# Performance work log

Measured on AMD Instinct MI355X. Metric: run time of the kernel, lower is better.

## Reference

```python
import jax, jax.numpy as jnp
import numpy as np
import math

N, E, G = 10000, 100000, 500
HID, H = 128, 4
C = HID                      # out_channels per head (PyG TransformerConv)
NFREQ, NSPACE = 10, 3
EDIM = 2 * NFREQ * NSPACE    # 60 = dis_emb.dim
LAT, DIS = 6, 3
IN_DIM = HID + LAT + DIS     # 137
EPS = 1e-5


def _lin_init(k, fan_in, shape):
    b = 1.0 / math.sqrt(fan_in)
    return jax.random.uniform(k, shape, jnp.float32, -b, b)


def setup_inputs() -> dict:
    key = jax.random.key(0)
    ks = jax.random.split(key, 12)
    return dict(
        node_features=jax.random.normal(ks[0], (N, HID), jnp.float32),
        frac_coords=jax.random.uniform(ks[1], (N, DIS), jnp.float32),
        lattice_feats=jax.random.normal(ks[2], (G, LAT), jnp.float32),
        edge_index=jax.random.randint(ks[3], (2, E), 0, N),
        node2graph=jnp.sort(jax.random.randint(ks[4], (N,), 0, G)),
        frac_diff=jax.random.normal(ks[5], (E, DIS), jnp.float32) * 0.1,
        ln_gamma=jnp.ones((HID,), jnp.float32),
        ln_beta=jnp.zeros((HID,), jnp.float32),
        Wq=_lin_init(ks[6], IN_DIM, (IN_DIM, H * C)), bq=jnp.zeros((H * C,), jnp.float32),
        Wk=_lin_init(ks[7], IN_DIM, (IN_DIM, H * C)), bk=jnp.zeros((H * C,), jnp.float32),
        Wv=_lin_init(ks[8], IN_DIM, (IN_DIM, H * C)), bv=jnp.zeros((H * C,), jnp.float32),
        We=_lin_init(ks[9], EDIM, (EDIM, H * C)),
        Wskip=_lin_init(ks[10], IN_DIM, (IN_DIM, C)), bskip=jnp.zeros((C,), jnp.float32),
    )


def _sinusoids(frac_diff):
    # SinusoidsEmbedding: emb = x[...,None]*2*pi*arange(F); cat(sin, cos); detached
    freqs = 2.0 * jnp.pi * jnp.arange(NFREQ, dtype=jnp.float32)    # [F]
    emb = frac_diff[:, :, None] * freqs[None, None, :]             # [E,3,F]
    emb = emb.reshape(-1, NSPACE * NFREQ)                          # [E,30]
    return jnp.concatenate([jnp.sin(emb), jnp.cos(emb)], axis=-1)  # [E,60]


def _segment_softmax(scores, idx, num_segments):
    # softmax over variable-size neighborhoods grouped by target node idx
    m = jax.ops.segment_max(scores, idx, num_segments=num_segments)
    ex = jnp.exp(scores - m[idx])
    s = jax.ops.segment_sum(ex, idx, num_segments=num_segments)
    return ex / (s[idx] + 1e-16)


def reference(node_features, frac_coords, lattice_feats, edge_index, node2graph,
              frac_diff, ln_gamma, ln_beta, Wq, bq, Wk, bk, Wv, bv, We, Wskip, bskip):
    edge_emb = jax.lax.stop_gradient(_sinusoids(frac_diff))  # .detach() in original
    node_input = node_features
    # LayerNorm (biased variance, torch default)
    mu = node_features.mean(-1, keepdims=True)
    var = node_features.var(-1, keepdims=True)
    h = (node_features - mu) * jax.lax.rsqrt(var + EPS) * ln_gamma + ln_beta
    # gather per-graph lattice features to nodes, concat
    lat = lattice_feats.reshape(-1, LAT)[node2graph]                # [N,6]
    x = jnp.concatenate([h, lat, frac_coords], axis=1)              # [N,137]

    q = (x @ Wq + bq).reshape(N, H, C)
    k = (x @ Wk + bk).reshape(N, H, C)
    v = (x @ Wv + bv).reshape(N, H, C)
    e = (edge_emb @ We).reshape(E, H, C)                            # lin_edge (no bias)

    src, dst = edge_index[0], edge_index[1]  # message flows src -> dst (PyG default)
    k_e = k[src] + e                                                # [E,H,C]
    alpha = (q[dst] * k_e).sum(-1) / math.sqrt(C)                   # [E,H]
    alpha = _segment_softmax(alpha, dst, N)
    msg = (v[src] + e) * alpha[:, :, None]                          # [E,H,C]
    out = jax.ops.segment_sum(msg, dst, num_segments=N)             # [N,H,C]
    out = out.mean(axis=1)                                          # concat=False -> head mean
    out = out + (x @ Wskip + bskip)                                 # root skip connection
    return node_input + jax.nn.silu(out)
```

## Files before the change

### kernel.cpp

```cpp
#include <hip/hip_runtime.h>
#include <math.h>

#define N_NODES 10000
#define N_EDGES 100000
#define HIDDEN  128
#define NHEAD   4
#define CHAN    128
#define IN_DIM  137
#define KPAD    160
#define NCOLS   1904
#define NPAD    1920
#define LATD    6
#define DISD    3

#define PREP_BLOCKS 2500
#define TRANS_TILES 26
#define WQE_BLOCKS  150
#define WEBT_BLOCKS 128

#define SCAT_BLOCKS ((N_EDGES + 255) / 256)
#define GEMM_BX 15
#define GEMM_BY ((N_NODES + 63) / 64)

typedef __attribute__((ext_vector_type(8))) short short8v;
typedef __attribute__((ext_vector_type(4))) float float4v;
typedef __attribute__((ext_vector_type(2))) float float2v;

__device__ inline unsigned short f2bf(float f) {
    unsigned u = __float_as_uint(f);
    unsigned r = 0x7fffu + ((u >> 16) & 1u);
    return (unsigned short)((u + r) >> 16);
}
__device__ inline float bf2f(unsigned short u) {
    return __uint_as_float(((unsigned)u) << 16);
}

__global__ __launch_bounds__(256) void prep_weights_kernel(
    const float* __restrict__ nf, const float* __restrict__ frac,
    const float* __restrict__ lat, const int* __restrict__ n2g,
    const float* __restrict__ gamma, const float* __restrict__ beta,
    const float* __restrict__ Wq, const float* __restrict__ bq,
    const float* __restrict__ Wk, const float* __restrict__ bk,
    const float* __restrict__ Wv, const float* __restrict__ bv,
    const float* __restrict__ Wsk, const float* __restrict__ bsk,
    const float* __restrict__ We,
    unsigned short* __restrict__ xb, int* __restrict__ hist,
    unsigned short* __restrict__ wallT, float* __restrict__ bias_all,
    unsigned short* __restrict__ webt)
{
    __shared__ __align__(16) unsigned short Tlds[64 * 168];
    const int tid = threadIdx.x;

    if (blockIdx.x < PREP_BLOCKS) {
        int wave = tid >> 6;
        int lane = tid & 63;
        int n = blockIdx.x * 4 + wave;
        if (n >= N_NODES) return;

        float v0 = nf[n * HIDDEN + lane];
        float v1 = nf[n * HIDDEN + 64 + lane];
        float s  = v0 + v1;
        float sq = v0 * v0 + v1 * v1;
        #pragma unroll
        for (int m = 1; m < 64; m <<= 1) {
            s  += __shfl_xor(s, m);
            sq += __shfl_xor(sq, m);
        }
        float mean = s * (1.0f / 128.0f);
        float var  = sq * (1.0f / 128.0f) - mean * mean;
        float inv  = rsqrtf(var + 1e-5f);

        xb[n * KPAD + lane]      = f2bf((v0 - mean) * inv * gamma[lane]      + beta[lane]);
        xb[n * KPAD + 64 + lane] = f2bf((v1 - mean) * inv * gamma[64 + lane] + beta[64 + lane]);
        if (lane < LATD) xb[n * KPAD + HIDDEN + lane]        = f2bf(lat[n2g[n] * LATD + lane]);
        if (lane < DISD) xb[n * KPAD + HIDDEN + LATD + lane] = f2bf(frac[n * DISD + lane]);
        if (lane >= 41)  xb[n * KPAD + 96 + lane] = 0;
        if (lane == 0)   hist[n] = 0;
    } else if (blockIdx.x < PREP_BLOCKS + TRANS_TILES) {
        const int n0 = (blockIdx.x - PREP_BLOCKS) * 64;
        for (int i = tid; i < 160 * 64; i += 256) {
            const int k = i >> 6, n = i & 63;
            const int col = n0 + n;
            float val = 0.0f;
            if (k < IN_DIM) {
                if (col < 512)        val = Wq[(size_t)k * 512 + col];
                else if (col < 1024)  val = Wk[(size_t)k * 512 + (col - 512)];
                else if (col < 1536)  val = Wv[(size_t)k * 512 + (col - 1024)];
                else                  val = Wsk[(size_t)k * 128 + (col - 1536)];
            }
            Tlds[n * 168 + k] = f2bf(val);
        }
        __syncthreads();
        for (int i = tid; i < 64 * 20; i += 256) {
            const int n = i / 20, c8 = (i % 20) * 8;
            *reinterpret_cast<uint4*>(&wallT[(size_t)(n0 + n) * KPAD + c8]) =
                *reinterpret_cast<const uint4*>(&Tlds[n * 168 + c8]);
        }
        if (tid < 64) {
            const int col = n0 + tid;
            float b;
            if (col < 512)        b = bq[col];
            else if (col < 1024)  b = bk[col - 512];
            else if (col < 1536)  b = bv[col - 1024];
            else                  b = bsk[col - 1536];
            bias_all[col] = b;
        }
    } else if (blockIdx.x < PREP_BLOCKS + TRANS_TILES + WQE_BLOCKS) {
        int idx = (blockIdx.x - PREP_BLOCKS - TRANS_TILES) * 256 + tid;
        if (idx >= 240 * KPAD) return;
        int hj = idx / KPAD, k = idx % KPAD;
        int h = hj / 60, j = hj % 60;
        float s = 0.0f;
        if (k < IN_DIM) {
            #pragma unroll 4
            for (int c = 0; c < 128; ++c)
                s += Wq[(size_t)k * 512 + h * 128 + c] * We[(size_t)j * 512 + h * 128 + c];
        }
        wallT[(size_t)(1664 + hj) * KPAD + k] = f2bf(s);
        if (k == KPAD - 1) {
            float b = 0.0f;
            #pragma unroll 4
            for (int c = 0; c < 128; ++c)
                b += bq[h * 128 + c] * We[(size_t)j * 512 + h * 128 + c];
            bias_all[1664 + hj] = b;
        }
    } else {
        int g = (blockIdx.x - PREP_BLOCKS - TRANS_TILES - WQE_BLOCKS) * 256 + tid;
        if (g >= 4 * 128 * 64) return;
        int h = g >> 13, c = (g >> 6) & 127, j = g & 63;
        float v = (j < 60) ? We[(size_t)j * 512 + h * 128 + c] : 0.0f;
        webt[g] = f2bf(v);
    }
}

__global__ __launch_bounds__(256) void hist_kernel(
    const int* __restrict__ eidx, int* __restrict__ hist)
{
    int e = blockIdx.x * 256 + threadIdx.x;
    if (e < N_EDGES) atomicAdd(&hist[eidx[N_EDGES + e]], 1);
}

__global__ __launch_bounds__(1024) void scan_kernel(
    const int* __restrict__ hist, int* __restrict__ offsets, int* __restrict__ cursor)
{
    __shared__ int part[1024];
    const int t = threadIdx.x;
    const int base = t * 10;
    int loc[10];
    int s = 0;
    #pragma unroll
    for (int i = 0; i < 10; ++i) {
        int v = (base + i < N_NODES) ? hist[base + i] : 0;
        loc[i] = s; s += v;
    }
    part[t] = s;
    __syncthreads();
    for (int off = 1; off < 1024; off <<= 1) {
        int v = (t >= off) ? part[t - off] : 0;
        __syncthreads();
        part[t] += v;
        __syncthreads();
    }
    int pre = (t > 0) ? part[t - 1] : 0;
    #pragma unroll
    for (int i = 0; i < 10; ++i)
        if (base + i < N_NODES) {
            offsets[base + i] = pre + loc[i];
            cursor[base + i]  = pre + loc[i];
        }
    if (t == 1023) offsets[N_NODES] = part[1023];
}

__global__ __launch_bounds__(256) void gemm_scatter_kernel(
    const unsigned short* __restrict__ xb, const unsigned short* __restrict__ wallT,
    const float* __restrict__ bias_all,
    const int* __restrict__ eidx, const float* __restrict__ fdiff,
    int* __restrict__ cursor, int* __restrict__ sorted_src,
    float* __restrict__ sorted_fd,
    float* __restrict__ sq, unsigned short* __restrict__ qbuf,
    unsigned char* __restrict__ kvb)
{
    __shared__ __align__(16) unsigned short Alds[64 * 168];

    if (blockIdx.x < SCAT_BLOCKS) {
        int e = blockIdx.x * 256 + threadIdx.x;
        if (e >= N_EDGES) return;
        int src = eidx[e];
        int dst = eidx[N_EDGES + e];
        int pos = atomicAdd(&cursor[dst], 1);
        sorted_src[pos] = src;
        sorted_fd[pos * 3 + 0] = fdiff[e * 3 + 0];
        sorted_fd[pos * 3 + 1] = fdiff[e * 3 + 1];
        sorted_fd[pos * 3 + 2] = fdiff[e * 3 + 2];
        return;
    }

    const int bx   = blockIdx.x - SCAT_BLOCKS;
    const int row0 = (bx / GEMM_BX) * 64;
    const int col0 = (bx % GEMM_BX) * 128;
    const int tid  = threadIdx.x;

    for (int i = tid; i < 64 * 20; i += 256) {
        int r = i / 20, c8 = (i % 20) * 8;
        uint4 v = make_uint4(0u, 0u, 0u, 0u);
        if (row0 + r < N_NODES)
            v = *reinterpret_cast<const uint4*>(&xb[(size_t)(row0 + r) * KPAD + c8]);
        *reinterpret_cast<uint4*>(&Alds[r * 168 + c8]) = v;
    }
    __syncthreads();

    const int l   = tid & 63;
    const int wid = tid >> 6;
    const int wr  = (wid >> 1) * 32;
    const int wc  = (wid & 1) * 64;
    const int lr  = l & 15;
    const int lk  = (l >> 4) * 8;

    float4v acc[2][4];
    #pragma unroll
    for (int tr = 0; tr < 2; ++tr)
        #pragma unroll
        for (int tc = 0; tc < 4; ++tc)
            acc[tr][tc] = (float4v){0.0f, 0.0f, 0.0f, 0.0f};

    #pragma unroll
    for (int ks = 0; ks < 5; ++ks) {
        short8v a[2], b[4];
        #pragma unroll
        for (int t = 0; t < 2; ++t)
            a[t] = *reinterpret_cast<const short8v*>(&Alds[(wr + t * 16 + lr) * 168 + ks * 32 + lk]);
        #pragma unroll
        for (int t = 0; t < 4; ++t)
            b[t] = *reinterpret_cast<const short8v*>(
                &wallT[(size_t)(col0 + wc + t * 16 + lr) * KPAD + ks * 32 + lk]);
        #pragma unroll
        for (int tr = 0; tr < 2; ++tr)
            #pragma unroll
            for (int tc = 0; tc < 4; ++tc)
                acc[tr][tc] = __builtin_amdgcn_mfma_f32_16x16x32_bf16(a[tr], b[tc], acc[tr][tc], 0, 0, 0);
    }

    #pragma unroll
    for (int tr = 0; tr < 2; ++tr) {
        #pragma unroll
        for (int tc = 0; tc < 4; ++tc) {
            const int col  = col0 + wc + tc * 16 + lr;
            const float bias = bias_all[col];
            #pragma unroll
            for (int j = 0; j < 4; ++j) {
                const int row = row0 + wr + tr * 16 + (l >> 4) * 4 + j;
                if (row < N_NODES) {
                    float val = acc[tr][tc][j] + bias;
                    if (col < 512) {
                        qbuf[(size_t)row * 512 + col] = f2bf(val);
                    } else if (col < 1024) {
                        const int h = (col - 512) >> 7, ck = (col - 512) & 127;
                        int p = __builtin_amdgcn_cvt_pk_fp8_f32(val, val, 0, false);
                        kvb[((size_t)row * 4 + h) * 256 + ck] = (unsigned char)(p & 0xFF);
                    } else if (col < 1536) {
                        const int h = (col - 1024) >> 7, cv = (col - 1024) & 127;
                        int p = __builtin_amdgcn_cvt_pk_fp8_f32(val, val, 0, false);
                        kvb[((size_t)row * 4 + h) * 256 + 128 + cv] = (unsigned char)(p & 0xFF);
                    } else if (col < 1664) {
                        sq[(size_t)row * 384 + (col - 1536)] = val;
                    } else if (col < NCOLS) {
                        sq[(size_t)row * 384 + 128 + (col - 1664)] = val;
                    }
                }
            }
        }
    }
}

__global__ __launch_bounds__(256) void gather_kernel(
    const float* __restrict__ sq, const unsigned short* __restrict__ qbuf,
    const unsigned char* __restrict__ kvb,
    const int* __restrict__ offsets, const int* __restrict__ sorted_src,
    const float* __restrict__ sorted_fd,
    float* __restrict__ avbuf, unsigned short* __restrict__ aggbuf,
    float* __restrict__ sumwbuf)
{
    const int n    = blockIdx.x;
    const int h    = threadIdx.x >> 6;
    const int l    = threadIdx.x & 63;
    const int hl   = l & 31;
    const int half = l >> 5;
    const float TWO_PI = 6.283185307179586f;
    const float scale  = 0.08838834764831845f;

    const ushort4 qv = *reinterpret_cast<const ushort4*>(
        &qbuf[(size_t)n * 512 + h * 128 + 4 * hl]);
    const float q4x = bf2f(qv.x), q4y = bf2f(qv.y);
    const float q4z = bf2f(qv.z), q4w = bf2f(qv.w);
    const float qe_a = sq[(size_t)n * 384 + 128 + h * 60 + hl];
    const bool  v2ok = (hl < 28);
    const float qe_b = v2ok ? sq[(size_t)n * 384 + 128 + h * 60 + hl + 32] : 0.0f;

    const int   jj1  = (hl < 30) ? hl : hl - 30;
    const int   sd1  = jj1 / 10;
    const float fc1  = TWO_PI * (float)(jj1 % 10);
    const bool  sin1 = (hl < 30);
    const int   jj2  = hl + 2;
    const int   sd2  = v2ok ? (jj2 / 10) : 0;
    const float fc2  = v2ok ? TWO_PI * (float)(jj2 % 10) : 0.0f;

    float ax = 0.f, ay = 0.f, az = 0.f, aw = 0.f;
    float agg1 = 0.f, agg2 = 0.f, sumw = 0.f;
    const int e0 = offsets[n], e1 = offsets[n + 1];

    for (int base = e0; base < e1; base += 4) {
        const int eA = base + half;
        const int eB = base + half + 2;
        const bool okA = (eA < e1), okB = (eB < e1);
        const int iA = okA ? eA : e0;
        const int iB = okB ? eB : e0;
        const int srcA = sorted_src[iA];
        const int srcB = sorted_src[iB];
        const float fdA1 = sorted_fd[iA * 3 + sd1];
        const float fdA2 = sorted_fd[iA * 3 + sd2];
        const float fdB1 = sorted_fd[iB * 3 + sd1];
        const float fdB2 = sorted_fd[iB * 3 + sd2];
        const unsigned char* pA = kvb + ((size_t)srcA * 4 + h) * 256;
        const unsigned char* pB = kvb + ((size_t)srcB * 4 + h) * 256;
        const unsigned kAu = *reinterpret_cast<const unsigned*>(pA + 4 * hl);
        const unsigned vAu = *reinterpret_cast<const unsigned*>(pA + 128 + 4 * hl);
        const unsigned kBu = *reinterpret_cast<const unsigned*>(pB + 4 * hl);
        const unsigned vBu = *reinterpret_cast<const unsigned*>(pB + 128 + 4 * hl);

        const float eA1 = sin1 ? __sinf(fdA1 * fc1) : __cosf(fdA1 * fc1);
        const float eA2 = __cosf(fdA2 * fc2);
        const float eB1 = sin1 ? __sinf(fdB1 * fc1) : __cosf(fdB1 * fc1);
        const float eB2 = __cosf(fdB2 * fc2);

        const float2v kA01 = __builtin_amdgcn_cvt_pk_f32_fp8(kAu, false);
        const float2v kA23 = __builtin_amdgcn_cvt_pk_f32_fp8(kAu, true);
        const float2v kB01 = __builtin_amdgcn_cvt_pk_f32_fp8(kBu, false);
        const float2v kB23 = __builtin_amdgcn_cvt_pk_f32_fp8(kBu, true);

        float pAs = q4x * kA01[0] + q4y * kA01[1]
                  + q4z * kA23[0] + q4w * kA23[1]
                  + eA1 * qe_a + eA2 * qe_b;
        float pBs = q4x * kB01[0] + q4y * kB01[1]
                  + q4z * kB23[0] + q4w * kB23[1]
                  + eB1 * qe_a + eB2 * qe_b;
        #pragma unroll
        for (int m = 1; m <= 16; m <<= 1) {
            pAs += __shfl_xor(pAs, m);
            pBs += __shfl_xor(pBs, m);
        }
        const float wA = okA ? __expf(pAs * scale) : 0.0f;
        const float wB = okB ? __expf(pBs * scale) : 0.0f;
        sumw += wA + wB;

        const float2v vA01 = __builtin_amdgcn_cvt_pk_f32_fp8(vAu, false);
        const float2v vA23 = __builtin_amdgcn_cvt_pk_f32_fp8(vAu, true);
        const float2v vB01 = __builtin_amdgcn_cvt_pk_f32_fp8(vBu, false);
        const float2v vB23 = __builtin_amdgcn_cvt_pk_f32_fp8(vBu, true);
        ax += wA * vA01[0] + wB * vB01[0];
        ay += wA * vA01[1] + wB * vB01[1];
        az += wA * vA23[0] + wB * vB23[0];
        aw += wA * vA23[1] + wB * vB23[1];
        agg1 += wA * eA1 + wB * eB1;
        if (v2ok) agg2 += wA * eA2 + wB * eB2;
    }

    sumw += __shfl_xor(sumw, 32);
    ax += __shfl_xor(ax, 32);  ay += __shfl_xor(ay, 32);
    az += __shfl_xor(az, 32);  aw += __shfl_xor(aw, 32);
    agg1 += __shfl_xor(agg1, 32);
    agg2 += __shfl_xor(agg2, 32);

    if (half == 0) {
        float4 r;
        r.x = ax; r.y = ay; r.z = az; r.w = aw;
        *reinterpret_cast<float4*>(&avbuf[(size_t)n * 512 + h * 128 + 4 * hl]) = r;
        aggbuf[n * 256 + h * 64 + hl]      = f2bf(agg1);
        aggbuf[n * 256 + h * 64 + 32 + hl] = f2bf(agg2);
        if (hl == 0) sumwbuf[n * 4 + h] = sumw;
    }
}

__global__ __launch_bounds__(256) void corr_kernel(
    const unsigned short* __restrict__ webt, const unsigned short* __restrict__ aggbuf,
    float* __restrict__ avbuf)
{
    __shared__ __align__(16) unsigned short Alds[32 * 264];
    const int node0 = blockIdx.x * 32;
    const int tid = threadIdx.x;

    for (int i = tid; i < 32 * 32; i += 256) {
        int r = i >> 5, c8 = (i & 31) * 8;
        uint4 v = make_uint4(0u, 0u, 0u, 0u);
        if (node0 + r < N_NODES)
            v = *reinterpret_cast<const uint4*>(&aggbuf[(size_t)(node0 + r) * 256 + c8]);
        *reinterpret_cast<uint4*>(&Alds[r * 264 + c8]) = v;
    }
    __syncthreads();

    const int l  = tid & 63;
    const int h  = tid >> 6;
    const int lr = l & 15;
    const int lk = (l >> 4) * 8;

    float4v acc[2][8];
    #pragma unroll
    for (int m = 0; m < 2; ++m)
        #pragma unroll
        for (int nn = 0; nn < 8; ++nn)
            acc[m][nn] = (float4v){0.0f, 0.0f, 0.0f, 0.0f};

    #pragma unroll
    for (int ks = 0; ks < 2; ++ks) {
        short8v a[2], b[8];
        #pragma unroll
        for (int m = 0; m < 2; ++m)
            a[m] = *reinterpret_cast<const short8v*>(
                &Alds[(m * 16 + lr) * 264 + h * 64 + ks * 32 + lk]);
        #pragma unroll
        for (int nn = 0; nn < 8; ++nn)
            b[nn] = *reinterpret_cast<const short8v*>(
                &webt[(size_t)(h * 128 + nn * 16 + lr) * 64 + ks * 32 + lk]);
        #pragma unroll
        for (int m = 0; m < 2; ++m)
            #pragma unroll
            for (int nn = 0; nn < 8; ++nn)
                acc[m][nn] = __builtin_amdgcn_mfma_f32_16x16x32_bf16(a[m], b[nn], acc[m][nn], 0, 0, 0);
    }

    #pragma unroll
    for (int m = 0; m < 2; ++m) {
        #pragma unroll
        for (int nn = 0; nn < 8; ++nn) {
            const int col = h * 128 + nn * 16 + lr;
            #pragma unroll
            for (int j = 0; j < 4; ++j) {
                const int rowi = node0 + m * 16 + (l >> 4) * 4 + j;
                if (rowi < N_NODES) {
                    float* p = &avbuf[(size_t)rowi * 512 + col];
                    *p += acc[m][nn][j];
                }
            }
        }
    }
}

__global__ __launch_bounds__(256) void finalize_kernel(
    const float* __restrict__ avbuf, const float* __restrict__ sumwbuf,
    const float* __restrict__ sq, const float* __restrict__ nf,
    float* __restrict__ out)
{
    int idx = blockIdx.x * 256 + threadIdx.x;
    if (idx >= N_NODES * CHAN) return;
    int n = idx >> 7, c = idx & 127;
    float z = 0.0f;
    #pragma unroll
    for (int h = 0; h < NHEAD; ++h)
        z += avbuf[(size_t)n * 512 + h * 128 + c] / (sumwbuf[n * 4 + h] + 1e-16f);
    z = 0.25f * z + sq[(size_t)n * 384 + c];
    float si = z / (1.0f + __expf(-z));
    out[idx] = nf[idx] + si;
}

extern "C" void kernel_launch(void* const* d_in, const int* in_sizes, int n_in,
                              void* d_out, int out_size, void* d_ws, size_t ws_size,
                              hipStream_t stream)
{
    const float* nf    = (const float*)d_in[0];
    const float* frac  = (const float*)d_in[1];
    const float* lat   = (const float*)d_in[2];
    const int*   eidx  = (const int*)  d_in[3];
    const int*   n2g   = (const int*)  d_in[4];
    const float* fdiff = (const float*)d_in[5];
    const float* gamma = (const float*)d_in[6];
    const float* beta  = (const float*)d_in[7];
    const float* Wq    = (const float*)d_in[8];
    const float* bq    = (const float*)d_in[9];
    const float* Wk    = (const float*)d_in[10];
    const float* bk    = (const float*)d_in[11];
    const float* Wv    = (const float*)d_in[12];
    const float* bv    = (const float*)d_in[13];
    const float* We    = (const float*)d_in[14];
    const float* Wsk   = (const float*)d_in[15];
    const float* bsk   = (const float*)d_in[16];
    float* out = (float*)d_out;

    float* sq        = (float*)d_ws;
    float* avbuf     = sq + (size_t)N_NODES * 384;
    float* sumwbuf   = avbuf + (size_t)N_NODES * 512;
    float* bias_all  = sumwbuf + (size_t)N_NODES * 4;
    float* sorted_fd = bias_all + NPAD;
    unsigned short* xb     = (unsigned short*)(sorted_fd + (size_t)N_EDGES * 3);
    unsigned short* wallT  = xb + (size_t)N_NODES * KPAD;
    unsigned short* webt   = wallT + (size_t)NPAD * KPAD;
    unsigned short* aggbuf = webt + 4 * 128 * 64;
    unsigned short* qbuf   = aggbuf + (size_t)N_NODES * 256;
    unsigned char*  kvb    = (unsigned char*)(qbuf + (size_t)N_NODES * 512);
    int* hist       = (int*)(kvb + (size_t)N_NODES * 4 * 256);
    int* offsets    = hist + N_NODES;
    int* cursor     = offsets + N_NODES + 1;
    int* sorted_src = cursor + N_NODES;

    prep_weights_kernel<<<PREP_BLOCKS + TRANS_TILES + WQE_BLOCKS + WEBT_BLOCKS,
                          256, 0, stream>>>(
        nf, frac, lat, n2g, gamma, beta,
        Wq, bq, Wk, bk, Wv, bv, Wsk, bsk, We,
        xb, hist, wallT, bias_all, webt);

    hist_kernel<<<(N_EDGES + 255) / 256, 256, 0, stream>>>(eidx, hist);
    scan_kernel<<<1, 1024, 0, stream>>>(hist, offsets, cursor);

    gemm_scatter_kernel<<<SCAT_BLOCKS + GEMM_BX * GEMM_BY, 256, 0, stream>>>(
        xb, wallT, bias_all, eidx, fdiff, cursor, sorted_src, sorted_fd,
        sq, qbuf, kvb);

    gather_kernel<<<N_NODES, 256, 0, stream>>>(
        sq, qbuf, kvb, offsets, sorted_src, sorted_fd, avbuf, aggbuf, sumwbuf);

    corr_kernel<<<(N_NODES + 31) / 32, 256, 0, stream>>>(webt, aggbuf, avbuf);

    finalize_kernel<<<(N_NODES * CHAN + 255) / 256, 256, 0, stream>>>(
        avbuf, sumwbuf, sq, nf, out);
}
```

Baseline: 141.1 us.

## Fuse histogram into single-block scan and merge correction with finalize

Replaces the global-atomic histogram kernel plus scan kernel with one single-block kernel that builds the destination histogram in LDS and scans it, removing a launch and the hist zeroing. Fuses the bf16 MFMA edge-embedding correction with the finalize step, so the correction is added in registers instead of read-modify-written into avbuf. Each wave now handles 16 nodes across all four heads. The risk is that the single block processes all 100k edges serially on one CU, and the fused kernel reads avbuf, sq and nf with a less coalesced per-lane pattern.

```diff
diff --git a/kernel.cpp b/kernel.cpp
--- a/kernel.cpp
+++ b/kernel.cpp
@@ -44,7 +44,7 @@
     const float* __restrict__ Wv, const float* __restrict__ bv,
     const float* __restrict__ Wsk, const float* __restrict__ bsk,
     const float* __restrict__ We,
-    unsigned short* __restrict__ xb, int* __restrict__ hist,
+    unsigned short* __restrict__ xb,
     unsigned short* __restrict__ wallT, float* __restrict__ bias_all,
     unsigned short* __restrict__ webt)
 {
@@ -75,7 +75,6 @@
         if (lane < LATD) xb[n * KPAD + HIDDEN + lane]        = f2bf(lat[n2g[n] * LATD + lane]);
         if (lane < DISD) xb[n * KPAD + HIDDEN + LATD + lane] = f2bf(frac[n * DISD + lane]);
         if (lane >= 41)  xb[n * KPAD + 96 + lane] = 0;
-        if (lane == 0)   hist[n] = 0;
     } else if (blockIdx.x < PREP_BLOCKS + TRANS_TILES) {
         const int n0 = (blockIdx.x - PREP_BLOCKS) * 64;
         for (int i = tid; i < 160 * 64; i += 256) {
@@ -133,24 +132,24 @@
     }
 }
 
-__global__ __launch_bounds__(256) void hist_kernel(
-    const int* __restrict__ eidx, int* __restrict__ hist)
+__global__ __launch_bounds__(1024) void histscan_kernel(
+    const int* __restrict__ eidx, int* __restrict__ offsets, int* __restrict__ cursor)
 {
-    int e = blockIdx.x * 256 + threadIdx.x;
-    if (e < N_EDGES) atomicAdd(&hist[eidx[N_EDGES + e]], 1);
-}
-
-__global__ __launch_bounds__(1024) void scan_kernel(
-    const int* __restrict__ hist, int* __restrict__ offsets, int* __restrict__ cursor)
-{
+    __shared__ int lhist[N_NODES];
     __shared__ int part[1024];
     const int t = threadIdx.x;
+    for (int i = t; i < N_NODES; i += 1024) lhist[i] = 0;
+    __syncthreads();
+    for (int e = t; e < N_EDGES; e += 1024)
+        atomicAdd(&lhist[eidx[N_EDGES + e]], 1);
+    __syncthreads();
+
     const int base = t * 10;
     int loc[10];
     int s = 0;
     #pragma unroll
     for (int i = 0; i < 10; ++i) {
-        int v = (base + i < N_NODES) ? hist[base + i] : 0;
+        int v = (base + i < N_NODES) ? lhist[base + i] : 0;
         loc[i] = s; s += v;
     }
     part[t] = s;
@@ -380,85 +379,71 @@
     }
 }
 
-__global__ __launch_bounds__(256) void corr_kernel(
+__global__ __launch_bounds__(256) void corrfin_kernel(
     const unsigned short* __restrict__ webt, const unsigned short* __restrict__ aggbuf,
-    float* __restrict__ avbuf)
-{
-    __shared__ __align__(16) unsigned short Alds[32 * 264];
-    const int node0 = blockIdx.x * 32;
-    const int tid = threadIdx.x;
-
-    for (int i = tid; i < 32 * 32; i += 256) {
-        int r = i >> 5, c8 = (i & 31) * 8;
-        uint4 v = make_uint4(0u, 0u, 0u, 0u);
-        if (node0 + r < N_NODES)
-            v = *reinterpret_cast<const uint4*>(&aggbuf[(size_t)(node0 + r) * 256 + c8]);
-        *reinterpret_cast<uint4*>(&Alds[r * 264 + c8]) = v;
-    }
-    __syncthreads();
-
-    const int l  = tid & 63;
-    const int h  = tid >> 6;
-    const int lr = l & 15;
-    const int lk = (l >> 4) * 8;
-
-    float4v acc[2][8];
-    #pragma unroll
-    for (int m = 0; m < 2; ++m)
-        #pragma unroll
-        for (int nn = 0; nn < 8; ++nn)
-            acc[m][nn] = (float4v){0.0f, 0.0f, 0.0f, 0.0f};
-
-    #pragma unroll
-    for (int ks = 0; ks < 2; ++ks) {
-        short8v a[2], b[8];
-        #pragma unroll
-        for (int m = 0; m < 2; ++m)
-            a[m] = *reinterpret_cast<const short8v*>(
-                &Alds[(m * 16 + lr) * 264 + h * 64 + ks * 32 + lk]);
-        #pragma unroll
-        for (int nn = 0; nn < 8; ++nn)
-            b[nn] = *reinterpret_cast<const short8v*>(
-                &webt[(size_t)(h * 128 + nn * 16 + lr) * 64 + ks * 32 + lk]);
-        #pragma unroll
-        for (int m = 0; m < 2; ++m)
-            #pragma unroll
-            for (int nn = 0; nn < 8; ++nn)
-                acc[m][nn] = __builtin_amdgcn_mfma_f32_16x16x32_bf16(a[m], b[nn], acc[m][nn], 0, 0, 0);
-    }
-
-    #pragma unroll
-    for (int m = 0; m < 2; ++m) {
-        #pragma unroll
-        for (int nn = 0; nn < 8; ++nn) {
-            const int col = h * 128 + nn * 16 + lr;
-            #pragma unroll
-            for (int j = 0; j < 4; ++j) {
-                const int rowi = node0 + m * 16 + (l >> 4) * 4 + j;
-                if (rowi < N_NODES) {
-                    float* p = &avbuf[(size_t)rowi * 512 + col];
-                    *p += acc[m][nn][j];
-                }
-            }
-        }
-    }
-}
-
-__global__ __launch_bounds__(256) void finalize_kernel(
     const float* __restrict__ avbuf, const float* __restrict__ sumwbuf,
     const float* __restrict__ sq, const float* __restrict__ nf,
     float* __restrict__ out)
 {
-    int idx = blockIdx.x * 256 + threadIdx.x;
-    if (idx >= N_NODES * CHAN) return;
-    int n = idx >> 7, c = idx & 127;
-    float z = 0.0f;
-    #pragma unroll
-    for (int h = 0; h < NHEAD; ++h)
-        z += avbuf[(size_t)n * 512 + h * 128 + c] / (sumwbuf[n * 4 + h] + 1e-16f);
-    z = 0.25f * z + sq[(size_t)n * 384 + c];
-    float si = z / (1.0f + __expf(-z));
-    out[idx] = nf[idx] + si;
+    const int node0 = blockIdx.x * 64;
+    const int tid = threadIdx.x;
+    const int l   = tid & 63;
+    const int w   = tid >> 6;
+    const int lr  = l & 15;
+    const int lk  = (l >> 4) * 8;
+    const int nbase = node0 + w * 16;
+
+    float4v acc[4][8];
+    #pragma unroll
+    for (int h = 0; h < 4; ++h)
+        #pragma unroll
+        for (int nn = 0; nn < 8; ++nn)
+            acc[h][nn] = (float4v){0.0f, 0.0f, 0.0f, 0.0f};
+
+    const int arow = (nbase + lr < N_NODES) ? (nbase + lr) : 0;
+    #pragma unroll
+    for (int h = 0; h < 4; ++h) {
+        #pragma unroll
+        for (int ks = 0; ks < 2; ++ks) {
+            const short8v a = *reinterpret_cast<const short8v*>(
+                &aggbuf[(size_t)arow * 256 + h * 64 + ks * 32 + lk]);
+            #pragma unroll
+            for (int nn = 0; nn < 8; ++nn) {
+                const short8v b = *reinterpret_cast<const short8v*>(
+                    &webt[(size_t)(h * 128 + nn * 16 + lr) * 64 + ks * 32 + lk]);
+                acc[h][nn] = __builtin_amdgcn_mfma_f32_16x16x32_bf16(a, b, acc[h][nn], 0, 0, 0);
+            }
+        }
+    }
+
+    float inv_sw[4][4];
+    #pragma unroll
+    for (int j = 0; j < 4; ++j) {
+        const int node = nbase + (l >> 4) * 4 + j;
+        const int nrd  = (node < N_NODES) ? node : 0;
+        #pragma unroll
+        for (int h = 0; h < 4; ++h)
+            inv_sw[j][h] = 1.0f / (sumwbuf[nrd * 4 + h] + 1e-16f);
+    }
+
+    #pragma unroll
+    for (int nn = 0; nn < 8; ++nn) {
+        const int col = nn * 16 + lr;
+        #pragma unroll
+        for (int j = 0; j < 4; ++j) {
+            const int node = nbase + (l >> 4) * 4 + j;
+            if (node < N_NODES) {
+                float z = 0.0f;
+                #pragma unroll
+                for (int h = 0; h < 4; ++h)
+                    z += (avbuf[(size_t)node * 512 + h * 128 + col] + acc[h][nn][j])
+                         * inv_sw[j][h];
+                z = 0.25f * z + sq[(size_t)node * 384 + col];
+                float si = z / (1.0f + __expf(-z));
+                out[node * CHAN + col] = nf[node * CHAN + col] + si;
+            }
+        }
+    }
 }
 
 extern "C" void kernel_launch(void* const* d_in, const int* in_sizes, int n_in,
@@ -495,8 +480,7 @@
     unsigned short* aggbuf = webt + 4 * 128 * 64;
     unsigned short* qbuf   = aggbuf + (size_t)N_NODES * 256;
     unsigned char*  kvb    = (unsigned char*)(qbuf + (size_t)N_NODES * 512);
-    int* hist       = (int*)(kvb + (size_t)N_NODES * 4 * 256);
-    int* offsets    = hist + N_NODES;
+    int* offsets    = (int*)(kvb + (size_t)N_NODES * 4 * 256);
     int* cursor     = offsets + N_NODES + 1;
     int* sorted_src = cursor + N_NODES;
 
@@ -504,10 +488,9 @@
                           256, 0, stream>>>(
         nf, frac, lat, n2g, gamma, beta,
         Wq, bq, Wk, bk, Wv, bv, Wsk, bsk, We,
-        xb, hist, wallT, bias_all, webt);
-
-    hist_kernel<<<(N_EDGES + 255) / 256, 256, 0, stream>>>(eidx, hist);
-    scan_kernel<<<1, 1024, 0, stream>>>(hist, offsets, cursor);
+        xb, wallT, bias_all, webt);
+
+    histscan_kernel<<<1, 1024, 0, stream>>>(eidx, offsets, cursor);
 
     gemm_scatter_kernel<<<SCAT_BLOCKS + GEMM_BX * GEMM_BY, 256, 0, stream>>>(
         xb, wallT, bias_all, eidx, fdiff, cursor, sorted_src, sorted_fd,
@@ -516,8 +499,6 @@
     gather_kernel<<<N_NODES, 256, 0, stream>>>(
         sq, qbuf, kvb, offsets, sorted_src, sorted_fd, avbuf, aggbuf, sumwbuf);
 
-    corr_kernel<<<(N_NODES + 31) / 32, 256, 0, stream>>>(webt, aggbuf, avbuf);
-
-    finalize_kernel<<<(N_NODES * CHAN + 255) / 256, 256, 0, stream>>>(
-        avbuf, sumwbuf, sq, nf, out);
-}
+    corrfin_kernel<<<(N_NODES + 63) / 64, 256, 0, stream>>>(
+        webt, aggbuf, avbuf, sumwbuf, sq, nf, out);
+}
```

Measured after the change: 151.8 us. 7.6% more time.
